# Optimization experiments

Measured on AMD Instinct MI355X. Metric: run time of the kernel, lower is better.

## Reference

```python
import jax, jax.numpy as jnp
import numpy as np

B = 4096
V = 50257
K = 64
LABEL_SMOOTHING = 0.1


def setup_inputs() -> dict:
    key = jax.random.key(0)
    k1, k2 = jax.random.split(key)
    inp = jax.random.normal(k1, (B, V), dtype=jnp.float32)
    target = jax.random.randint(k2, (B,), 0, V, dtype=jnp.int64)
    return {"input": inp, "target": target}


def reference(input, target):
    rows = jnp.arange(input.shape[0])
    # gather the true-class logit: (B, 1)
    truth = input[rows, target][:, None]
    # mask the true class to -inf so top-k selects k hardest negatives
    masked = input.at[rows, target].set(-jnp.inf)
    topk_vals = jax.lax.top_k(masked, K)[0]          # (B, K)
    selected = jnp.concatenate([truth, topk_vals], axis=-1)  # (B, K+1)
    # cross-entropy with target class 0 and label smoothing (torch semantics:
    # loss = (1-eps)*nll + eps * mean_c(-log p_c))
    logp = jax.nn.log_softmax(selected, axis=-1)
    nll = -logp[:, 0]
    smooth = -jnp.mean(logp, axis=-1)
    per_ex = (1.0 - LABEL_SMOOTHING) * nll + LABEL_SMOOTHING * smooth
    return jnp.mean(per_ex)
```

## Files before the change

kernel.cpp:

```cpp
#include <hip/hip_runtime.h>
#include <math.h>
#include <stdint.h>

#define BROWS 4096
#define VCOLS 50257
#define KTOP  64
#define CAP   2048
#define CHECK_AT 1024
#define NREG 32

__device__ __forceinline__ unsigned f2key(float f) {
    unsigned u = __float_as_uint(f);
    return u ^ ((unsigned)((int)u >> 31) | 0x80000000u);
}
__device__ __forceinline__ float key2f(unsigned k) {
    unsigned u = (k & 0x80000000u) ? (k ^ 0x80000000u) : ~k;
    return __uint_as_float(u);
}

__device__ __forceinline__ int wave_sum_i(int c) {
    #pragma unroll
    for (int d = 1; d < 64; d <<= 1) c += __shfl_xor(c, d);
    return c;
}

__device__ __forceinline__ void load_keys(const float* s_buf, unsigned cnt, int lane, unsigned* key) {
    #pragma unroll
    for (int j = 0; j < NREG / 4; ++j) {
        const float4 v = ((const float4*)s_buf)[j * 64 + lane];
        const int base = (j * 64 + lane) * 4;
        key[4*j+0] = (base + 0 < (int)cnt) ? f2key(v.x) : 0u;
        key[4*j+1] = (base + 1 < (int)cnt) ? f2key(v.y) : 0u;
        key[4*j+2] = (base + 2 < (int)cnt) ? f2key(v.z) : 0u;
        key[4*j+3] = (base + 3 < (int)cnt) ? f2key(v.w) : 0u;
    }
}

__device__ __attribute__((noinline)) unsigned long long
wave_compact_f(float* s_buf, unsigned cnt, unsigned lo_in, int lane) {
    __builtin_amdgcn_wave_barrier();
    unsigned key[NREG];
    load_keys(s_buf, cnt, lane, key);
    unsigned kmx = 0u;
    #pragma unroll
    for (int j = 0; j < NREG; ++j) kmx = max(kmx, key[j]);
    #pragma unroll
    for (int d = 1; d < 64; d <<= 1) kmx = max(kmx, (unsigned)__shfl_xor((int)kmx, d));

    unsigned lo = lo_in;
    unsigned hi = kmx + 1u;
    for (int it = 0; it < 12; ++it) {
        if (hi - lo <= 1u) break;
        const unsigned mid = lo + ((hi - lo) >> 1);
        int c = 0;
        #pragma unroll
        for (int j = 0; j < NREG; ++j) c += (key[j] >= mid) ? 1 : 0;
        c = wave_sum_i(c);
        if (c >= KTOP) lo = mid; else hi = mid;
    }
    int cl = 0; unsigned sm = 0u;
    #pragma unroll
    for (int j = 0; j < NREG; ++j) { const bool s = key[j] >= lo; sm |= (unsigned)s << j; cl += s ? 1 : 0; }
    int incl = cl;
    #pragma unroll
    for (int d = 1; d < 64; d <<= 1) { const int t = __shfl_up(incl, d); if (lane >= d) incl += t; }
    int pos = incl - cl;
    __builtin_amdgcn_wave_barrier();
    #pragma unroll
    for (int j = 0; j < NREG; ++j) if ((sm >> j) & 1u) s_buf[pos++] = key2f(key[j]);
    const unsigned ncnt = (unsigned)__shfl(incl, 63);
    __builtin_amdgcn_wave_barrier();
    return ((unsigned long long)ncnt << 32) | (unsigned long long)lo;
}

__device__ __forceinline__ float wave_final(const float* s_buf, unsigned cnt, float thr, float tv, int lane) {
    __builtin_amdgcn_wave_barrier();
    unsigned key[NREG];
    load_keys(s_buf, cnt, lane, key);
    unsigned kmx = 0u;
    #pragma unroll
    for (int j = 0; j < NREG; ++j) kmx = max(kmx, key[j]);
    #pragma unroll
    for (int d = 1; d < 64; d <<= 1) kmx = max(kmx, (unsigned)__shfl_xor((int)kmx, d));

    unsigned lo = f2key(thr);
    unsigned hi = kmx + 1u;
    while (hi - lo > 1u) {
        const unsigned mid = lo + ((hi - lo) >> 1);
        int c = 0;
        #pragma unroll
        for (int j = 0; j < NREG; ++j) c += (key[j] >= mid) ? 1 : 0;
        c = wave_sum_i(c);
        if (c >= KTOP) lo = mid; else hi = mid;
    }
    const float vmax = key2f(kmx);
    const float m = fmaxf(vmax, tv);
    float se = 0.f, sv = 0.f; int cg = 0;
    #pragma unroll
    for (int j = 0; j < NREG; ++j) {
        if (key[j] > lo) { const float v = key2f(key[j]); se += __expf(v - m); sv += v; ++cg; }
    }
    #pragma unroll
    for (int d = 1; d < 64; d <<= 1) {
        se += __shfl_xor(se, d); sv += __shfl_xor(sv, d); cg += __shfl_xor(cg, d);
    }
    const float v64 = key2f(lo);
    const int nb = KTOP - cg;
    se += (float)nb * __expf(v64 - m);
    sv += (float)nb * v64;
    se += __expf(tv - m);
    const float lse = m + __logf(se);
    return lse - 0.9f * tv - 0.1f * ((sv + tv) * (1.0f / 65.0f));
}

__device__ __forceinline__ void ins1(float v, int gi, int tgt, float thr,
                                     float* s_buf, unsigned& cnt, unsigned long long lt) {
    const bool p = (v > thr) && (gi != tgt);
    const unsigned long long mk = __ballot(p ? 1 : 0);
    if (mk) {
        if (p) {
            const unsigned pos = cnt + (unsigned)__popcll(mk & lt);
            if (pos < CAP) s_buf[pos] = v;
        }
        cnt += (unsigned)__popcll(mk);
    }
}
__device__ __forceinline__ void ins4(const float4 q, int gb, int tgt, float thr,
                                     float* s_buf, unsigned& cnt, unsigned long long lt) {
    ins1(q.x, gb + 0, tgt, thr, s_buf, cnt, lt);
    ins1(q.y, gb + 1, tgt, thr, s_buf, cnt, lt);
    ins1(q.z, gb + 2, tgt, thr, s_buf, cnt, lt);
    ins1(q.w, gb + 3, tgt, thr, s_buf, cnt, lt);
}

#define LOADT(A0,A1,A2,A3, tq) do { const int b_ = (tq)*256 + lane; \
    A0 = vp[b_]; A1 = vp[b_+64]; A2 = vp[b_+128]; A3 = vp[b_+192]; } while (0)

#define PROC(A0,A1,A2,A3, tq) do { \
    const int bq_ = (tq)*256 + lane; \
    const float mA_ = fmaxf(fmaxf(A0.x,A0.y), fmaxf(A0.z,A0.w)); \
    const float mB_ = fmaxf(fmaxf(A1.x,A1.y), fmaxf(A1.z,A1.w)); \
    const float mC_ = fmaxf(fmaxf(A2.x,A2.y), fmaxf(A2.z,A2.w)); \
    const float mD_ = fmaxf(fmaxf(A3.x,A3.y), fmaxf(A3.z,A3.w)); \
    const float m16_ = fmaxf(fmaxf(mA_,mB_), fmaxf(mC_,mD_)); \
    if (__ballot((m16_ > thr) ? 1 : 0)) { \
        ins4(A0, pad + 4*bq_,       tgt, thr, s_buf, cnt, lt); \
        ins4(A1, pad + 4*(bq_+64),  tgt, thr, s_buf, cnt, lt); \
        ins4(A2, pad + 4*(bq_+128), tgt, thr, s_buf, cnt, lt); \
        ins4(A3, pad + 4*(bq_+192), tgt, thr, s_buf, cnt, lt); \
    } \
    if (cnt > CHECK_AT) { \
        const unsigned long long r_ = wave_compact_f(s_buf, cnt, f2key(thr), lane); \
        cnt = (unsigned)(r_ >> 32); thr = key2f((unsigned)r_); \
    } \
} while (0)

__global__ __launch_bounds__(64) void topk_ce_kernel(
        const float* __restrict__ input, const int* __restrict__ target,
        float* __restrict__ per_ex, float* __restrict__ out_atomic) {
    __shared__ float s_buf[CAP];
    const int row  = blockIdx.x;
    const int lane = threadIdx.x;
    const float* __restrict__ rowp = input + (size_t)row * (size_t)VCOLS;
    const int tgt = target[row];
    const float tv = rowp[tgt];
    const unsigned long long lt = (1ull << lane) - 1ull;

    unsigned cnt = 0u;
    float thr = -INFINITY;

    const int pad = (int)((4u - ((((uintptr_t)rowp) >> 2) & 3u)) & 3u);
    {
        const float v = (lane < pad) ? rowp[lane] : 0.f;
        const bool p = (lane < pad) && (lane != tgt);
        const unsigned long long mk = __ballot(p ? 1 : 0);
        if (p) s_buf[cnt + __popcll(mk & lt)] = v;
        cnt += (unsigned)__popcll(mk);
    }

    const int nvec  = (VCOLS - pad) >> 2;
    const int ntail = (VCOLS - pad) & 3;
    const float4* __restrict__ vp = (const float4*)(rowp + pad);
    const int ntf = nvec >> 8;

    float4 a0, a1, a2, a3, b0, b1, b2, b3;
    int t = 0;
    if (ntf > 0) LOADT(a0, a1, a2, a3, 0);
    for (; t + 2 <= ntf; t += 2) {
        LOADT(b0, b1, b2, b3, t + 1);
        PROC(a0, a1, a2, a3, t);
        if (t + 2 < ntf) LOADT(a0, a1, a2, a3, t + 2);
        PROC(b0, b1, b2, b3, t + 1);
    }
    if (t < ntf) PROC(a0, a1, a2, a3, t);

    for (int k0 = ntf * 256; k0 < nvec; k0 += 64) {
        const int idx = k0 + lane;
        float4 a;
        if (idx < nvec) a = vp[idx];
        else { a.x = a.y = a.z = a.w = -INFINITY; }
        const float mA = fmaxf(fmaxf(a.x, a.y), fmaxf(a.z, a.w));
        if (__ballot((mA > thr) ? 1 : 0)) ins4(a, pad + 4 * idx, tgt, thr, s_buf, cnt, lt);
        if (cnt > CHECK_AT) {
            const unsigned long long r = wave_compact_f(s_buf, cnt, f2key(thr), lane);
            cnt = (unsigned)(r >> 32); thr = key2f((unsigned)r);
        }
    }

    {
        const int idx = pad + 4 * nvec + lane;
        const float v = (lane < ntail) ? rowp[idx] : 0.f;
        const bool p = (lane < ntail) && (v > thr) && (idx != tgt);
        const unsigned long long mk = __ballot(p ? 1 : 0);
        if (p) {
            const unsigned pos = cnt + (unsigned)__popcll(mk & lt);
            if (pos < CAP) s_buf[pos] = v;
        }
        cnt += (unsigned)__popcll(mk);
    }

    const float pe = wave_final(s_buf, cnt, thr, tv, lane);
    if (lane == 0) {
        if (per_ex) per_ex[row] = pe;
        else atomicAdd(out_atomic, pe * (1.0f / BROWS));
    }
}

__global__ __launch_bounds__(256) void reduce_mean_kernel(
        const float* __restrict__ per_ex, float* __restrict__ out) {
    __shared__ float s[256];
    const int tid = threadIdx.x;
    float acc = 0.0f;
    for (int i = tid; i < BROWS; i += 256) acc += per_ex[i];
    s[tid] = acc;
    __syncthreads();
    for (int w = 128; w > 0; w >>= 1) {
        if (tid < w) s[tid] += s[tid + w];
        __syncthreads();
    }
    if (tid == 0) out[0] = s[0] * (1.0f / BROWS);
}

extern "C" void kernel_launch(void* const* d_in, const int* in_sizes, int n_in,
                              void* d_out, int out_size, void* d_ws, size_t ws_size,
                              hipStream_t stream) {
    const float* input  = (const float*)d_in[0];
    const int*   target = (const int*)d_in[1];
    float* out = (float*)d_out;

    if (ws_size >= BROWS * sizeof(float)) {
        float* per_ex = (float*)d_ws;
        topk_ce_kernel<<<BROWS, 64, 0, stream>>>(input, target, per_ex, nullptr);
        reduce_mean_kernel<<<1, 256, 0, stream>>>(per_ex, out);
    } else {
        hipMemsetAsync(d_out, 0, sizeof(float), stream);
        topk_ce_kernel<<<BROWS, 64, 0, stream>>>(input, target, nullptr, out);
    }
}
```

Baseline: 184.0 us.

## Seed threshold from first tile, inline compaction, fuse final mean via last-block reduction

Processes the first 1024 elements of each row up front by radix-searching a top-64 threshold and seeding the candidate buffer. Later tiles can then reject most values at once instead of filling the buffer from -inf and compacting. The compaction routine is force-inlined instead of noinline, and the separate reduce kernel is replaced by an atomic counter so the last finishing block computes the mean. This adds a memset launch for the counter and more register pressure from inlining.

Result: slower. 306.2 us (+66.4%).

```diff
diff --git a/kernel.cpp b/kernel.cpp
--- a/kernel.cpp
+++ b/kernel.cpp
@@ -36,8 +36,7 @@
     }
 }
 
-__device__ __attribute__((noinline)) unsigned long long
-wave_compact_f(float* s_buf, unsigned cnt, unsigned lo_in, int lane) {
+__device__ __forceinline__ void wave_compact(float* s_buf, unsigned& cnt, float& thr, int lane) {
     __builtin_amdgcn_wave_barrier();
     unsigned key[NREG];
     load_keys(s_buf, cnt, lane, key);
@@ -47,7 +46,7 @@
     #pragma unroll
     for (int d = 1; d < 64; d <<= 1) kmx = max(kmx, (unsigned)__shfl_xor((int)kmx, d));
 
-    unsigned lo = lo_in;
+    unsigned lo = f2key(thr);
     unsigned hi = kmx + 1u;
     for (int it = 0; it < 12; ++it) {
         if (hi - lo <= 1u) break;
@@ -68,9 +67,9 @@
     __builtin_amdgcn_wave_barrier();
     #pragma unroll
     for (int j = 0; j < NREG; ++j) if ((sm >> j) & 1u) s_buf[pos++] = key2f(key[j]);
-    const unsigned ncnt = (unsigned)__shfl(incl, 63);
+    cnt = (unsigned)__shfl(incl, 63);
+    thr = key2f(lo);
     __builtin_amdgcn_wave_barrier();
-    return ((unsigned long long)ncnt << 32) | (unsigned long long)lo;
 }
 
 __device__ __forceinline__ float wave_final(const float* s_buf, unsigned cnt, float thr, float tv, int lane) {
@@ -149,15 +148,13 @@
         ins4(A2, pad + 4*(bq_+128), tgt, thr, s_buf, cnt, lt); \
         ins4(A3, pad + 4*(bq_+192), tgt, thr, s_buf, cnt, lt); \
     } \
-    if (cnt > CHECK_AT) { \
-        const unsigned long long r_ = wave_compact_f(s_buf, cnt, f2key(thr), lane); \
-        cnt = (unsigned)(r_ >> 32); thr = key2f((unsigned)r_); \
-    } \
+    if (cnt > CHECK_AT) wave_compact(s_buf, cnt, thr, lane); \
 } while (0)
 
 __global__ __launch_bounds__(64) void topk_ce_kernel(
         const float* __restrict__ input, const int* __restrict__ target,
-        float* __restrict__ per_ex, float* __restrict__ out_atomic) {
+        float* __restrict__ per_ex, unsigned* __restrict__ counter,
+        float* __restrict__ out) {
     __shared__ float s_buf[CAP];
     const int row  = blockIdx.x;
     const int lane = threadIdx.x;
@@ -167,25 +164,81 @@
     const unsigned long long lt = (1ull << lane) - 1ull;
 
     unsigned cnt = 0u;
-    float thr = -INFINITY;
-
-    const int pad = (int)((4u - ((((uintptr_t)rowp) >> 2) & 3u)) & 3u);
-    {
-        const float v = (lane < pad) ? rowp[lane] : 0.f;
-        const bool p = (lane < pad) && (lane != tgt);
-        const unsigned long long mk = __ballot(p ? 1 : 0);
-        if (p) s_buf[cnt + __popcll(mk & lt)] = v;
-        cnt += (unsigned)__popcll(mk);
-    }
-
+    float thr;
+
+    const int pad   = (int)((4u - ((((uintptr_t)rowp) >> 2) & 3u)) & 3u);
     const int nvec  = (VCOLS - pad) >> 2;
     const int ntail = (VCOLS - pad) & 3;
     const float4* __restrict__ vp = (const float4*)(rowp + pad);
     const int ntf = nvec >> 8;
 
+    {
+        const int b = lane;
+        const float4 w0 = vp[b];
+        const float4 w1 = vp[b + 64];
+        const float4 w2 = vp[b + 128];
+        const float4 w3 = vp[b + 192];
+        unsigned k[16];
+        const int e0 = pad + 4 * b, e1 = pad + 4 * (b + 64),
+                  e2 = pad + 4 * (b + 128), e3 = pad + 4 * (b + 192);
+        k[0]  = (e0+0 != tgt) ? f2key(w0.x) : 0u;
+        k[1]  = (e0+1 != tgt) ? f2key(w0.y) : 0u;
+        k[2]  = (e0+2 != tgt) ? f2key(w0.z) : 0u;
+        k[3]  = (e0+3 != tgt) ? f2key(w0.w) : 0u;
+        k[4]  = (e1+0 != tgt) ? f2key(w1.x) : 0u;
+        k[5]  = (e1+1 != tgt) ? f2key(w1.y) : 0u;
+        k[6]  = (e1+2 != tgt) ? f2key(w1.z) : 0u;
+        k[7]  = (e1+3 != tgt) ? f2key(w1.w) : 0u;
+        k[8]  = (e2+0 != tgt) ? f2key(w2.x) : 0u;
+        k[9]  = (e2+1 != tgt) ? f2key(w2.y) : 0u;
+        k[10] = (e2+2 != tgt) ? f2key(w2.z) : 0u;
+        k[11] = (e2+3 != tgt) ? f2key(w2.w) : 0u;
+        k[12] = (e3+0 != tgt) ? f2key(w3.x) : 0u;
+        k[13] = (e3+1 != tgt) ? f2key(w3.y) : 0u;
+        k[14] = (e3+2 != tgt) ? f2key(w3.z) : 0u;
+        k[15] = (e3+3 != tgt) ? f2key(w3.w) : 0u;
+        unsigned kmx = 0u;
+        #pragma unroll
+        for (int j = 0; j < 16; ++j) kmx = max(kmx, k[j]);
+        #pragma unroll
+        for (int d = 1; d < 64; d <<= 1) kmx = max(kmx, (unsigned)__shfl_xor((int)kmx, d));
+        unsigned lo = 0u, hi = kmx + 1u;
+        for (int it = 0; it < 12; ++it) {
+            if (hi - lo <= 1u) break;
+            const unsigned mid = lo + ((hi - lo) >> 1);
+            int c = 0;
+            #pragma unroll
+            for (int j = 0; j < 16; ++j) c += (k[j] >= mid) ? 1 : 0;
+            c = wave_sum_i(c);
+            if (c >= KTOP) lo = mid; else hi = mid;
+        }
+        int cl = 0; unsigned sm = 0u;
+        #pragma unroll
+        for (int j = 0; j < 16; ++j) { const bool s = k[j] >= lo; sm |= (unsigned)s << j; cl += s ? 1 : 0; }
+        int incl = cl;
+        #pragma unroll
+        for (int d = 1; d < 64; d <<= 1) { const int t = __shfl_up(incl, d); if (lane >= d) incl += t; }
+        int pos = incl - cl;
+        #pragma unroll
+        for (int j = 0; j < 16; ++j) if ((sm >> j) & 1u) s_buf[pos++] = key2f(k[j]);
+        cnt = (unsigned)__shfl(incl, 63);
+        thr = key2f(lo);
+    }
+
+    {
+        const float v = (lane < pad) ? rowp[lane] : 0.f;
+        const bool p = (lane < pad) && (v > thr) && (lane != tgt);
+        const unsigned long long mk = __ballot(p ? 1 : 0);
+        if (p) {
+            const unsigned pos = cnt + (unsigned)__popcll(mk & lt);
+            if (pos < CAP) s_buf[pos] = v;
+        }
+        cnt += (unsigned)__popcll(mk);
+    }
+
     float4 a0, a1, a2, a3, b0, b1, b2, b3;
-    int t = 0;
-    if (ntf > 0) LOADT(a0, a1, a2, a3, 0);
+    int t = 1;
+    if (t < ntf) LOADT(a0, a1, a2, a3, t);
     for (; t + 2 <= ntf; t += 2) {
         LOADT(b0, b1, b2, b3, t + 1);
         PROC(a0, a1, a2, a3, t);
@@ -194,17 +247,14 @@
     }
     if (t < ntf) PROC(a0, a1, a2, a3, t);
 
-    for (int k0 = ntf * 256; k0 < nvec; k0 += 64) {
+    for (int k0 = ntf << 8; k0 < nvec; k0 += 64) {
         const int idx = k0 + lane;
         float4 a;
         if (idx < nvec) a = vp[idx];
         else { a.x = a.y = a.z = a.w = -INFINITY; }
         const float mA = fmaxf(fmaxf(a.x, a.y), fmaxf(a.z, a.w));
         if (__ballot((mA > thr) ? 1 : 0)) ins4(a, pad + 4 * idx, tgt, thr, s_buf, cnt, lt);
-        if (cnt > CHECK_AT) {
-            const unsigned long long r = wave_compact_f(s_buf, cnt, f2key(thr), lane);
-            cnt = (unsigned)(r >> 32); thr = key2f((unsigned)r);
-        }
+        if (cnt > CHECK_AT) wave_compact(s_buf, cnt, thr, lane);
     }
 
     {
@@ -220,25 +270,31 @@
     }
 
     const float pe = wave_final(s_buf, cnt, thr, tv, lane);
-    if (lane == 0) {
-        if (per_ex) per_ex[row] = pe;
-        else atomicAdd(out_atomic, pe * (1.0f / BROWS));
-    }
-}
-
-__global__ __launch_bounds__(256) void reduce_mean_kernel(
-        const float* __restrict__ per_ex, float* __restrict__ out) {
-    __shared__ float s[256];
-    const int tid = threadIdx.x;
-    float acc = 0.0f;
-    for (int i = tid; i < BROWS; i += 256) acc += per_ex[i];
-    s[tid] = acc;
-    __syncthreads();
-    for (int w = 128; w > 0; w >>= 1) {
-        if (tid < w) s[tid] += s[tid + w];
-        __syncthreads();
-    }
-    if (tid == 0) out[0] = s[0] * (1.0f / BROWS);
+
+    if (per_ex) {
+        unsigned done = 0u;
+        if (lane == 0) {
+            per_ex[row] = pe;
+            __threadfence();
+            done = atomicAdd(counter, 1u);
+        }
+        done = (unsigned)__shfl((int)done, 0);
+        if (done == (unsigned)(BROWS - 1)) {
+            __threadfence();
+            const float4* p4 = (const float4*)per_ex;
+            float acc = 0.0f;
+            #pragma unroll
+            for (int i = 0; i < 16; ++i) {
+                const float4 q = p4[i * 64 + lane];
+                acc += (q.x + q.y) + (q.z + q.w);
+            }
+            #pragma unroll
+            for (int d = 1; d < 64; d <<= 1) acc += __shfl_xor(acc, d);
+            if (lane == 0) out[0] = acc * (1.0f / BROWS);
+        }
+    } else {
+        if (lane == 0) atomicAdd(out, pe * (1.0f / BROWS));
+    }
 }
 
 extern "C" void kernel_launch(void* const* d_in, const int* in_sizes, int n_in,
@@ -248,12 +304,15 @@
     const int*   target = (const int*)d_in[1];
     float* out = (float*)d_out;
 
-    if (ws_size >= BROWS * sizeof(float)) {
-        float* per_ex = (float*)d_ws;
-        topk_ce_kernel<<<BROWS, 64, 0, stream>>>(input, target, per_ex, nullptr);
-        reduce_mean_kernel<<<1, 256, 0, stream>>>(per_ex, out);
+    float*    per_ex  = (float*)d_ws;
+    unsigned* counter = (unsigned*)((char*)d_ws + BROWS * sizeof(float));
+    const size_t need = BROWS * sizeof(float) + sizeof(unsigned);
+
+    if (ws_size >= need) {
+        hipMemsetAsync(counter, 0, sizeof(unsigned), stream);
+        topk_ce_kernel<<<BROWS, 64, 0, stream>>>(input, target, per_ex, counter, out);
     } else {
         hipMemsetAsync(d_out, 0, sizeof(float), stream);
-        topk_ce_kernel<<<BROWS, 64, 0, stream>>>(input, target, nullptr, out);
-    }
-}
+        topk_ce_kernel<<<BROWS, 64, 0, stream>>>(input, target, nullptr, nullptr, out);
+    }
+}
```
